# Kernel tuning notes

Hardware: AMD Instinct MI355X
Metric: run time of the kernel (lower is better)

The kernel has to match this reference:

```python
import jax, jax.numpy as jnp
import numpy as np

N = 100_000      # nodes
E = 1_600_000    # edges
D = 128          # in_dim == hidden_dim
H = 4            # heads
HD = D // H      # per-head dim = 32
B = 8            # graphs in batch
TD = 128         # time_dim
NEG_SLOPE = 0.2
EPS = 1e-5


def _gelu(v):
    return jax.nn.gelu(v, approximate=False)  # torch default erf-GELU


def _layernorm(v, g, b):
    mu = jnp.mean(v, axis=-1, keepdims=True)
    var = jnp.var(v, axis=-1, keepdims=True)
    return (v - mu) * jax.lax.rsqrt(var + EPS) * g + b


def setup_inputs() -> dict:
    key = jax.random.key(0)
    ks = jax.random.split(key, 24)
    s = 1.0 / np.sqrt(D)
    inp = {
        "x": jax.random.normal(ks[0], (N, D), jnp.float32),
        "src": jax.random.randint(ks[1], (E,), 0, N),
        "dst": jax.random.randint(ks[2], (E,), 0, N),
        "graph_ids": jnp.sort(jax.random.randint(ks[3], (N,), 0, B)),
        "time_emb": jax.random.normal(ks[4], (B, TD), jnp.float32),
        # GATv2 params
        "Wsrc": jax.random.normal(ks[5], (D, D), jnp.float32) * s,
        "bsrc": jnp.zeros((D,), jnp.float32),
        "Wdst": jax.random.normal(ks[6], (D, D), jnp.float32) * s,
        "bdst": jnp.zeros((D,), jnp.float32),
        "attn": jax.random.normal(ks[7], (H, HD), jnp.float32) * (1.0 / np.sqrt(HD)),
        "gat_bias": jnp.zeros((D,), jnp.float32),
        # LayerNorms
        "ln1_g": jnp.ones((D,), jnp.float32), "ln1_b": jnp.zeros((D,), jnp.float32),
        "ln2_g": jnp.ones((D,), jnp.float32), "ln2_b": jnp.zeros((D,), jnp.float32),
        # time MLP
        "tW": jax.random.normal(ks[8], (TD, D), jnp.float32) * (1.0 / np.sqrt(TD)),
        "tb": jnp.zeros((D,), jnp.float32),
        # FFN
        "W1": jax.random.normal(ks[9], (D, 2 * D), jnp.float32) * s,
        "b1": jnp.zeros((2 * D,), jnp.float32),
        "W2": jax.random.normal(ks[10], (2 * D, D), jnp.float32) * (1.0 / np.sqrt(2 * D)),
        "b2": jnp.zeros((D,), jnp.float32),
    }
    return inp


def reference(x, src, dst, graph_ids, time_emb, Wsrc, bsrc, Wdst, bdst, attn,
              gat_bias, ln1_g, ln1_b, ln2_g, ln2_b, tW, tb, W1, b1, W2, b2):
    h = _layernorm(x, ln1_g, ln1_b)                       # [N, D]
    # GATv2Conv (share_weights=False, residual=False, activation=gelu)
    feat_src = (h @ Wsrc + bsrc).reshape(N, H, HD)        # [N, H, HD]
    feat_dst = (h @ Wdst + bdst).reshape(N, H, HD)
    e = feat_src[src] + feat_dst[dst]                     # [E, H, HD]
    e = jnp.where(e > 0, e, NEG_SLOPE * e)                # leaky_relu
    scores = jnp.einsum("ehd,hd->eh", e, attn)            # [E, H]
    # segment softmax over incoming edges of each dst node
    m = jax.ops.segment_max(scores, dst, num_segments=N)  # [N, H]
    ex = jnp.exp(scores - m[dst])
    denom = jax.ops.segment_sum(ex, dst, num_segments=N)  # [N, H]
    alpha = ex / denom[dst]                               # [E, H]
    msg = feat_src[src] * alpha[:, :, None]               # [E, H, HD]
    rst = jax.ops.segment_sum(msg, dst, num_segments=N)   # [N, H, HD]
    rst = _gelu(rst + gat_bias.reshape(H, HD))
    h = rst.reshape(N, D)                                 # flatten(1)
    # ragged time-embedding expand: time_condition[graph_of(node)]
    time_cond = _gelu(time_emb @ tW + tb)                 # [B, D]
    h = h + time_cond[graph_ids]
    h = h + x                                             # proj = Identity (in_dim == hidden_dim)
    h2 = _layernorm(h, ln2_g, ln2_b)
    h2 = _gelu(h2 @ W1 + b1) @ W2 + b2                    # FFN
    return h + h2
```

## Files before the change

### kernel.cpp

```cpp
#include <hip/hip_runtime.h>
#include <hip/hip_bf16.h>


#define RB 16
#define NEG_SLOPE 0.2f
#define LN_EPS 1e-5f

typedef __attribute__((ext_vector_type(8))) short short8v;
typedef __attribute__((ext_vector_type(4))) float floatx4;
typedef __attribute__((ext_vector_type(2))) float f32x2;

__device__ __forceinline__ float gelu_erf(float v) {
    return 0.5f * v * (1.0f + erff(v * 0.70710678118654752f));
}
__device__ __forceinline__ unsigned short f2bf(float f) {
    unsigned int u = __float_as_uint(f);
    u += 0x7fffu + ((u >> 16) & 1u);
    return (unsigned short)(u >> 16);
}
__device__ __forceinline__ float bf2f(unsigned short u) {
    return __uint_as_float(((unsigned int)u) << 16);
}

__device__ __forceinline__ void pack_region(
    const float* __restrict__ W, unsigned short* __restrict__ P, int K, int C, int idx)
{
    int total = (K >> 5) * (C >> 4) * 64;
    if (idx >= total) return;
    int lane = idx & 63;
    int f = idx >> 6;
    int nkt = K >> 5;
    int nt = f / nkt, kt = f - nt * nkt;
    int col = nt * 16 + (lane & 15);
    int k0 = kt * 32 + 8 * (lane >> 4);
    short8v v;
    #pragma unroll
    for (int i = 0; i < 8; ++i)
        v[i] = (short)f2bf(W[(size_t)(k0 + i) * C + col]);
    *(short8v*)(P + (size_t)idx * 8) = v;
}

__global__ __launch_bounds__(256) void prep(
    const int* __restrict__ dst, int* __restrict__ deg, int* __restrict__ rank,
    int E, int nRank,
    const float* __restrict__ temb, const float* __restrict__ tW,
    const float* __restrict__ tb, float* __restrict__ tc, int B,
    const float* __restrict__ Wsrc, unsigned short* __restrict__ pWs,
    const float* __restrict__ Wdst, unsigned short* __restrict__ pWd,
    const float* __restrict__ W1,   unsigned short* __restrict__ pW1,
    const float* __restrict__ W2,   unsigned short* __restrict__ pW2)
{
    const int t = threadIdx.x;
    if (blockIdx.x < nRank) {
        int e = blockIdx.x * 256 + t;
        if (e < E) rank[e] = atomicAdd(&deg[dst[e]], 1);
        return;
    }
    const int bid = blockIdx.x - nRank;
    if (bid == 0) {
        __shared__ float te[8 * 128];
        for (int i = t; i < B * 128; i += 256) te[i] = temb[i];
        __syncthreads();
        int c = t & 127, half = t >> 7;
        for (int b = half * 4; b < half * 4 + 4; ++b) {
            if (b >= B) break;
            float acc = 0.f;
            for (int k = 0; k < 128; ++k) acc = fmaf(te[b * 128 + k], tW[k * 128 + c], acc);
            tc[b * 128 + c] = gelu_erf(acc + tb[c]);
        }
    } else if (bid < 9) {
        pack_region(Wsrc, pWs, 128, 128, (bid - 1) * 256 + t);
    } else if (bid < 17) {
        pack_region(Wdst, pWd, 128, 128, (bid - 9) * 256 + t);
    } else if (bid < 33) {
        pack_region(W1, pW1, 128, 256, (bid - 17) * 256 + t);
    } else {
        pack_region(W2, pW2, 256, 128, (bid - 33) * 256 + t);
    }
}

__global__ __launch_bounds__(256) void scan_blocks(
    const int* __restrict__ deg, int* __restrict__ rs, int* __restrict__ btot, int N)
{
    __shared__ int wtot[4];
    const int t    = threadIdx.x;
    const int idx  = blockIdx.x * 1024 + t * 4;
    int d0 = 0, d1 = 0, d2 = 0, d3 = 0;
    if (idx + 3 < N) {
        int4 v = *(const int4*)(deg + idx);
        d0 = v.x; d1 = v.y; d2 = v.z; d3 = v.w;
    } else {
        if (idx     < N) d0 = deg[idx];
        if (idx + 1 < N) d1 = deg[idx + 1];
        if (idx + 2 < N) d2 = deg[idx + 2];
        if (idx + 3 < N) d3 = deg[idx + 3];
    }
    const int ts = d0 + d1 + d2 + d3;
    const int lane = t & 63, w = t >> 6;
    int incl = ts;
    #pragma unroll
    for (int m = 1; m < 64; m <<= 1) { int u = __shfl_up(incl, m); if (lane >= m) incl += u; }
    if (lane == 63) wtot[w] = incl;
    __syncthreads();
    int woff = 0;
    #pragma unroll
    for (int i = 0; i < 4; ++i) woff += (i < w) ? wtot[i] : 0;
    const int p = woff + incl - ts;
    if (idx + 3 < N) {
        int4 o;
        o.x = p; o.y = p + d0; o.z = p + d0 + d1; o.w = p + d0 + d1 + d2;
        *(int4*)(rs + idx) = o;
    } else {
        if (idx     < N) rs[idx]     = p;
        if (idx + 1 < N) rs[idx + 1] = p + d0;
        if (idx + 2 < N) rs[idx + 2] = p + d0 + d1;
        if (idx + 3 < N) rs[idx + 3] = p + d0 + d1 + d2;
    }
    if (t == 255) btot[blockIdx.x] = woff + incl;
}

__global__ __launch_bounds__(64) void scan_tops(
    int* __restrict__ btot, int nb, int* __restrict__ rs, int N, int E)
{
    const int lane = threadIdx.x;
    int a0 = (2 * lane     < nb) ? btot[2 * lane]     : 0;
    int a1 = (2 * lane + 1 < nb) ? btot[2 * lane + 1] : 0;
    const int ts = a0 + a1;
    int incl = ts;
    #pragma unroll
    for (int m = 1; m < 64; m <<= 1) { int u = __shfl_up(incl, m); if (lane >= m) incl += u; }
    const int ex = incl - ts;
    if (2 * lane     < nb) btot[2 * lane]     = ex;
    if (2 * lane + 1 < nb) btot[2 * lane + 1] = ex + a0;
    if (lane == 0) rs[N] = E;
}

__global__ __launch_bounds__(256) void scan_add(
    int* __restrict__ rs, const int* __restrict__ btot, int N)
{
    int i = blockIdx.x * 256 + threadIdx.x;
    if (i < N) rs[i] += btot[i >> 10];
}

__global__ __launch_bounds__(256) void ln1_fill(
    const float* __restrict__ x,
    const float* __restrict__ ln_g, const float* __restrict__ ln_b,
    const unsigned short* __restrict__ pWs, const float* __restrict__ bsrc,
    const unsigned short* __restrict__ pWd, const float* __restrict__ bdst,
    unsigned short* __restrict__ fs, unsigned short* __restrict__ fdB, int nrows, int nLn1,
    const int* __restrict__ dst, const int* __restrict__ srcA,
    const int* __restrict__ rs, const int* __restrict__ rank,
    int* __restrict__ srcSorted, int E)
{
    __shared__ __align__(16) float hs[RB][132];
    __shared__ __align__(16) unsigned short pa[4 * 64 * 8];
    __shared__ float s_mu[RB], s_rs[RB];

    if (blockIdx.x >= nLn1) {
        int e = (blockIdx.x - nLn1) * 256 + threadIdx.x;
        if (e < E) srcSorted[rs[dst[e]] + rank[e]] = srcA[e];
        return;
    }

    const int tid  = threadIdx.x;
    const int row0 = blockIdx.x * RB;
    const int lane = tid & 63;
    const int w    = tid >> 6;

    #pragma unroll
    for (int i = 0; i < 2; ++i) {
        int f   = tid + i * 256;
        int row = f >> 5;
        int c0  = (f & 31) * 4;
        float4 v = make_float4(0.f, 0.f, 0.f, 0.f);
        if (row0 + row < nrows) v = *(const float4*)(x + (size_t)(row0 + row) * 128 + c0);
        *(float4*)&hs[row][c0] = v;
    }
    __syncthreads();

    {
        const int ln = lane;
        #pragma unroll
        for (int rr = 0; rr < 4; ++rr) {
            int row = w * 4 + rr;
            float v0 = hs[row][ln * 2], v1 = hs[row][ln * 2 + 1];
            float s = v0 + v1, sq = v0 * v0 + v1 * v1;
            #pragma unroll
            for (int m = 32; m; m >>= 1) { s += __shfl_xor(s, m); sq += __shfl_xor(sq, m); }
            if (ln == 0) {
                float mu  = s * (1.0f / 128.0f);
                float var = sq * (1.0f / 128.0f) - mu * mu;
                s_mu[row] = mu;
                s_rs[row] = rsqrtf(var + LN_EPS);
            }
        }
    }
    __syncthreads();

    {
        const int kt  = w;
        const int row = lane & 15;
        const int k0  = kt * 32 + 8 * (lane >> 4);
        float mu = s_mu[row], rs2 = s_rs[row];
        float4 u  = *(float4*)&hs[row][k0];
        float4 v  = *(float4*)&hs[row][k0 + 4];
        float4 g0 = *(const float4*)&ln_g[k0];
        float4 g1 = *(const float4*)&ln_g[k0 + 4];
        float4 c0 = *(const float4*)&ln_b[k0];
        float4 c1 = *(const float4*)&ln_b[k0 + 4];
        short8v pv;
        pv[0] = (short)f2bf((u.x - mu) * rs2 * g0.x + c0.x);
        pv[1] = (short)f2bf((u.y - mu) * rs2 * g0.y + c0.y);
        pv[2] = (short)f2bf((u.z - mu) * rs2 * g0.z + c0.z);
        pv[3] = (short)f2bf((u.w - mu) * rs2 * g0.w + c0.w);
        pv[4] = (short)f2bf((v.x - mu) * rs2 * g1.x + c1.x);
        pv[5] = (short)f2bf((v.y - mu) * rs2 * g1.y + c1.y);
        pv[6] = (short)f2bf((v.z - mu) * rs2 * g1.z + c1.z);
        pv[7] = (short)f2bf((v.w - mu) * rs2 * g1.w + c1.w);
        *(short8v*)&pa[(kt * 64 + lane) * 8] = pv;
    }
    __syncthreads();

    short8v a[4];
    #pragma unroll
    for (int kt = 0; kt < 4; ++kt)
        a[kt] = *(const short8v*)&pa[(kt * 64 + lane) * 8];

    #pragma unroll
    for (int j = 0; j < 2; ++j) {
        const int nt = 2 * w + j;
        floatx4 aS = {0.f, 0.f, 0.f, 0.f};
        floatx4 aD = {0.f, 0.f, 0.f, 0.f};
        #pragma unroll
        for (int kt = 0; kt < 4; ++kt) {
            short8v bS = *(const short8v*)(pWs + (size_t)((nt * 4 + kt) * 64 + lane) * 8);
            aS = __builtin_amdgcn_mfma_f32_16x16x32_bf16(a[kt], bS, aS, 0, 0, 0);
            short8v bD = *(const short8v*)(pWd + (size_t)((nt * 4 + kt) * 64 + lane) * 8);
            aD = __builtin_amdgcn_mfma_f32_16x16x32_bf16(a[kt], bD, aD, 0, 0, 0);
        }
        const int col = nt * 16 + (lane & 15);
        const float bS0 = bsrc[col], bD0 = bdst[col];
        #pragma unroll
        for (int r = 0; r < 4; ++r) {
            int grow = row0 + 4 * (lane >> 4) + r;
            if (grow < nrows) {
                fs [(size_t)grow * 128 + col] = f2bf(aS[r] + bS0);
                fdB[(size_t)grow * 128 + col] = f2bf(aD[r] + bD0);
            }
        }
    }
}

__global__ __launch_bounds__(256) void gat_gather(
    const unsigned short* __restrict__ fs, const unsigned short* __restrict__ fdB,
    unsigned short* __restrict__ hm, const float* __restrict__ x,
    const int* __restrict__ srcSorted, const int* __restrict__ rs,
    const float* __restrict__ attn, const float* __restrict__ gat_bias,
    const int* __restrict__ gid, const float* __restrict__ tc, int N)
{
    const int lane = threadIdx.x & 63;
    const int wib  = threadIdx.x >> 6;
    const int n    = blockIdx.x * 4 + wib;
    if (n >= N) return;

    const int g   = lane >> 4;
    const int l16 = lane & 15;
    const int d0  = l16 * 8;

    f32x2 c1v[4], c2v[4], vdv[4];
    {
        float4 a0 = *(const float4*)(attn + d0);
        float4 a1 = *(const float4*)(attn + d0 + 4);
        float av[8] = {a0.x, a0.y, a0.z, a0.w, a1.x, a1.y, a1.z, a1.w};
        uint4 vdu = *(const uint4*)(fdB + (size_t)n * 128 + d0);
        unsigned int uu[4] = {vdu.x, vdu.y, vdu.z, vdu.w};
        #pragma unroll
        for (int j = 0; j < 4; ++j) {
            c1v[j].x = 0.6f * av[2 * j];     c1v[j].y = 0.6f * av[2 * j + 1];
            c2v[j].x = 0.4f * av[2 * j];     c2v[j].y = 0.4f * av[2 * j + 1];
            vdv[j].x = __uint_as_float(uu[j] << 16);
            vdv[j].y = __uint_as_float(uu[j] & 0xffff0000u);
        }
    }

    const int lo = rs[n], hi = rs[n + 1];
    const int T  = (hi - lo + 3) >> 2;

    float den = 0.f;
    f32x2 wv[4] = {{0.f, 0.f}, {0.f, 0.f}, {0.f, 0.f}, {0.f, 0.f}};

    int i = lo + g;
    bool vA = (i < hi);
    int sA = vA ? srcSorted[i] : 0;
    uint4 rA = *(const uint4*)(fs + (size_t)sA * 128 + d0);

    for (int t = 0; t < T; ++t) {
        const int inx = i + 4;
        const bool vB = (inx < hi);
        const int sB = vB ? srcSorted[inx] : 0;
        uint4 rB = *(const uint4*)(fs + (size_t)sB * 128 + d0);

        unsigned int ru[4] = {rA.x, rA.y, rA.z, rA.w};
        f32x2 v2[4];
        #pragma unroll
        for (int j = 0; j < 4; ++j) {
            v2[j].x = __uint_as_float(ru[j] << 16);
            v2[j].y = __uint_as_float(ru[j] & 0xffff0000u);
        }

        f32x2 p2 = {0.f, 0.f};
        #pragma unroll
        for (int j = 0; j < 4; ++j) {
            f32x2 e = v2[j] + vdv[j];
            p2 = __builtin_elementwise_fma(c1v[j], e, p2);
            p2 = __builtin_elementwise_fma(c2v[j],
                     __builtin_elementwise_abs(e), p2);
        }
        float p = p2.x + p2.y;
        p += __shfl_xor(p, 1);
        p += __shfl_xor(p, 2);
        float exv = vA ? __expf(p) : 0.f;
        den += exv;
        f32x2 ex2; ex2.x = exv; ex2.y = exv;
        #pragma unroll
        for (int j = 0; j < 4; ++j)
            wv[j] = __builtin_elementwise_fma(ex2, v2[j], wv[j]);

        vA = vB; rA = rB; i = inx;
    }

    float w[8];
    #pragma unroll
    for (int j = 0; j < 4; ++j) { w[2 * j] = wv[j].x; w[2 * j + 1] = wv[j].y; }

    den += __shfl_xor(den, 16);
    den += __shfl_xor(den, 32);
    #pragma unroll
    for (int j = 0; j < 8; ++j) {
        w[j] += __shfl_xor(w[j], 16);
        w[j] += __shfl_xor(w[j], 32);
    }

    if (g == 0) {
        const float inv = den > 0.f ? 1.0f / den : 0.f;
        const int gg = gid[n];
        float4 x0 = *(const float4*)(x  + (size_t)n * 128 + d0);
        float4 x1 = *(const float4*)(x  + (size_t)n * 128 + d0 + 4);
        float4 t0 = *(const float4*)(tc + (size_t)gg * 128 + d0);
        float4 t1 = *(const float4*)(tc + (size_t)gg * 128 + d0 + 4);
        float4 g0 = *(const float4*)(gat_bias + d0);
        float4 g1 = *(const float4*)(gat_bias + d0 + 4);
        float o[8];
        o[0] = gelu_erf(w[0] * inv + g0.x) + t0.x + x0.x;
        o[1] = gelu_erf(w[1] * inv + g0.y) + t0.y + x0.y;
        o[2] = gelu_erf(w[2] * inv + g0.z) + t0.z + x0.z;
        o[3] = gelu_erf(w[3] * inv + g0.w) + t0.w + x0.w;
        o[4] = gelu_erf(w[4] * inv + g1.x) + t1.x + x1.x;
        o[5] = gelu_erf(w[5] * inv + g1.y) + t1.y + x1.y;
        o[6] = gelu_erf(w[6] * inv + g1.z) + t1.z + x1.z;
        o[7] = gelu_erf(w[7] * inv + g1.w) + t1.w + x1.w;
        uint4 pk;
        pk.x = (unsigned int)f2bf(o[0]) | ((unsigned int)f2bf(o[1]) << 16);
        pk.y = (unsigned int)f2bf(o[2]) | ((unsigned int)f2bf(o[3]) << 16);
        pk.z = (unsigned int)f2bf(o[4]) | ((unsigned int)f2bf(o[5]) << 16);
        pk.w = (unsigned int)f2bf(o[6]) | ((unsigned int)f2bf(o[7]) << 16);
        *(uint4*)(hm + (size_t)n * 128 + d0) = pk;
    }
}

__global__ __launch_bounds__(256) void combine_ffn(
    const unsigned short* __restrict__ hmg,
    const float* __restrict__ ln_g, const float* __restrict__ ln_b,
    const unsigned short* __restrict__ pW1, const float* __restrict__ b1,
    const unsigned short* __restrict__ pW2, const float* __restrict__ b2,
    float* __restrict__ out, int nrows)
{
    __shared__ __align__(16) float hs[RB][132];
    __shared__ __align__(16) unsigned short pa[4 * 64 * 8];
    __shared__ __align__(16) unsigned short a2[RB * 264];
    __shared__ float s_mu[RB], s_rs[RB];

    const int tid  = threadIdx.x;
    const int row0 = blockIdx.x * RB;
    const int lane = tid & 63;
    const int w    = tid >> 6;

    {
        int row = tid >> 4;
        int c0  = (tid & 15) * 8;
        uint4 u = make_uint4(0, 0, 0, 0);
        if (row0 + row < nrows) u = *(const uint4*)(hmg + (size_t)(row0 + row) * 128 + c0);
        float* hr = &hs[row][c0];
        hr[0] = __uint_as_float(u.x << 16);
        hr[1] = __uint_as_float(u.x & 0xffff0000u);
        hr[2] = __uint_as_float(u.y << 16);
        hr[3] = __uint_as_float(u.y & 0xffff0000u);
        hr[4] = __uint_as_float(u.z << 16);
        hr[5] = __uint_as_float(u.z & 0xffff0000u);
        hr[6] = __uint_as_float(u.w << 16);
        hr[7] = __uint_as_float(u.w & 0xffff0000u);
    }
    __syncthreads();

    {
        const int ln = lane;
        #pragma unroll
        for (int rr = 0; rr < 4; ++rr) {
            int row = w * 4 + rr;
            float v0 = hs[row][ln * 2], v1 = hs[row][ln * 2 + 1];
            float s = v0 + v1, sq = v0 * v0 + v1 * v1;
            #pragma unroll
            for (int m = 32; m; m >>= 1) { s += __shfl_xor(s, m); sq += __shfl_xor(sq, m); }
            if (ln == 0) {
                float mu  = s * (1.0f / 128.0f);
                float var = sq * (1.0f / 128.0f) - mu * mu;
                s_mu[row] = mu;
                s_rs[row] = rsqrtf(var + LN_EPS);
            }
        }
    }
    __syncthreads();

    {
        const int kt  = w;
        const int row = lane & 15;
        const int k0  = kt * 32 + 8 * (lane >> 4);
        float mu = s_mu[row], rs2 = s_rs[row];
        float4 u  = *(float4*)&hs[row][k0];
        float4 v  = *(float4*)&hs[row][k0 + 4];
        float4 g0 = *(const float4*)&ln_g[k0];
        float4 g1 = *(const float4*)&ln_g[k0 + 4];
        float4 c0 = *(const float4*)&ln_b[k0];
        float4 c1 = *(const float4*)&ln_b[k0 + 4];
        short8v pv;
        pv[0] = (short)f2bf((u.x - mu) * rs2 * g0.x + c0.x);
        pv[1] = (short)f2bf((u.y - mu) * rs2 * g0.y + c0.y);
        pv[2] = (short)f2bf((u.z - mu) * rs2 * g0.z + c0.z);
        pv[3] = (short)f2bf((u.w - mu) * rs2 * g0.w + c0.w);
        pv[4] = (short)f2bf((v.x - mu) * rs2 * g1.x + c1.x);
        pv[5] = (short)f2bf((v.y - mu) * rs2 * g1.y + c1.y);
        pv[6] = (short)f2bf((v.z - mu) * rs2 * g1.z + c1.z);
        pv[7] = (short)f2bf((v.w - mu) * rs2 * g1.w + c1.w);
        *(short8v*)&pa[(kt * 64 + lane) * 8] = pv;
    }
    __syncthreads();

    {
        short8v a[4];
        #pragma unroll
        for (int kt = 0; kt < 4; ++kt)
            a[kt] = *(const short8v*)&pa[(kt * 64 + lane) * 8];

        #pragma unroll
        for (int jj = 0; jj < 4; ++jj) {
            const int nt = 4 * w + jj;
            floatx4 acc = {0.f, 0.f, 0.f, 0.f};
            #pragma unroll
            for (int kt = 0; kt < 4; ++kt) {
                short8v b = *(const short8v*)(pW1 + (size_t)((nt * 4 + kt) * 64 + lane) * 8);
                acc = __builtin_amdgcn_mfma_f32_16x16x32_bf16(a[kt], b, acc, 0, 0, 0);
            }
            const int col = nt * 16 + (lane & 15);
            const float bb = b1[col];
            #pragma unroll
            for (int r = 0; r < 4; ++r) {
                int rowD = 4 * (lane >> 4) + r;
                a2[rowD * 264 + col] = f2bf(gelu_erf(acc[r] + bb));
            }
        }
    }
    __syncthreads();

    {
        floatx4 acc2[2] = {{0.f, 0.f, 0.f, 0.f}, {0.f, 0.f, 0.f, 0.f}};
        #pragma unroll
        for (int kt = 0; kt < 8; ++kt) {
            short8v af = *(const short8v*)&a2[(lane & 15) * 264 + kt * 32 + 8 * (lane >> 4)];
            #pragma unroll
            for (int j = 0; j < 2; ++j) {
                const int nt = 2 * w + j;
                short8v b = *(const short8v*)(pW2 + (size_t)((nt * 8 + kt) * 64 + lane) * 8);
                acc2[j] = __builtin_amdgcn_mfma_f32_16x16x32_bf16(af, b, acc2[j], 0, 0, 0);
            }
        }
        #pragma unroll
        for (int j = 0; j < 2; ++j) {
            const int col = (2 * w + j) * 16 + (lane & 15);
            const float bb = b2[col];
            #pragma unroll
            for (int r = 0; r < 4; ++r) {
                int rowD = 4 * (lane >> 4) + r;
                int grow = row0 + rowD;
                if (grow < nrows)
                    out[(size_t)grow * 128 + col] = hs[rowD][col] + acc2[j][r] + bb;
            }
        }
    }
}

extern "C" void kernel_launch(void* const* d_in, const int* in_sizes, int n_in,
                              void* d_out, int out_size, void* d_ws, size_t ws_size,
                              hipStream_t stream)
{
    const float* x    = (const float*)d_in[0];
    const int*   src  = (const int*)  d_in[1];
    const int*   dst  = (const int*)  d_in[2];
    const int*   gid  = (const int*)  d_in[3];
    const float* temb = (const float*)d_in[4];
    const float* Wsrc = (const float*)d_in[5];
    const float* bsrc = (const float*)d_in[6];
    const float* Wdst = (const float*)d_in[7];
    const float* bdst = (const float*)d_in[8];
    const float* attn = (const float*)d_in[9];
    const float* gbias= (const float*)d_in[10];
    const float* ln1g = (const float*)d_in[11];
    const float* ln1b = (const float*)d_in[12];
    const float* ln2g = (const float*)d_in[13];
    const float* ln2b = (const float*)d_in[14];
    const float* tW   = (const float*)d_in[15];
    const float* tb   = (const float*)d_in[16];
    const float* W1   = (const float*)d_in[17];
    const float* b1   = (const float*)d_in[18];
    const float* W2   = (const float*)d_in[19];
    const float* b2   = (const float*)d_in[20];

    const int N = in_sizes[0] / 128;
    const int E = in_sizes[1];
    const int B = in_sizes[4] / 128;
    float* out = (float*)d_out;

    char* ws = (char*)d_ws;
    size_t off = 0;
    auto alloc = [&](size_t bytes) { void* p = ws + off; off += (bytes + 255) & ~(size_t)255; return p; };
    unsigned short* fs  = (unsigned short*)alloc((size_t)N * 128 * 2);
    unsigned short* fdB = (unsigned short*)alloc((size_t)N * 128 * 2);
    unsigned short* hm  = (unsigned short*)alloc((size_t)N * 128 * 2);
    int*   deg          = (int*)           alloc((size_t)N * 4);
    int*   rsb          = (int*)           alloc((size_t)(N + 1) * 4);
    int*   rank         = (int*)           alloc((size_t)E * 4);
    int*   srcSorted    = (int*)           alloc((size_t)E * 4);
    float* tc           = (float*)         alloc((size_t)B * 128 * 4);
    int*   btot         = (int*)           alloc((size_t)1024 * 4);
    unsigned short* pWs = (unsigned short*)alloc((size_t)128 * 128 * 2);
    unsigned short* pWd = (unsigned short*)alloc((size_t)128 * 128 * 2);
    unsigned short* pW1 = (unsigned short*)alloc((size_t)128 * 256 * 2);
    unsigned short* pW2 = (unsigned short*)alloc((size_t)256 * 128 * 2);

    const int nbScan = (N + 1023) >> 10;
    const int nRank  = (E + 255) / 256;
    const int nLn1   = (N + RB - 1) / RB;
    const int nFill  = (E + 255) / 256;

    hipMemsetAsync(deg, 0, (size_t)N * 4, stream);
    prep<<<nRank + 49, 256, 0, stream>>>(dst, deg, rank, E, nRank,
        temb, tW, tb, tc, B, Wsrc, pWs, Wdst, pWd, W1, pW1, W2, pW2);
    scan_blocks<<<nbScan, 256, 0, stream>>>(deg, rsb, btot, N);
    scan_tops<<<1, 64, 0, stream>>>(btot, nbScan, rsb, N, E);
    scan_add<<<(N + 255) / 256, 256, 0, stream>>>(rsb, btot, N);
    ln1_fill<<<nLn1 + nFill, 256, 0, stream>>>(
        x, ln1g, ln1b, pWs, bsrc, pWd, bdst, fs, fdB, N, nLn1,
        dst, src, rsb, rank, srcSorted, E);
    gat_gather<<<(N + 3) / 4, 256, 0, stream>>>(
        fs, fdB, hm, x, srcSorted, rsb, attn, gbias, gid, tc, N);
    combine_ffn<<<(N + RB - 1) / RB, 256, 0, stream>>>(
        hm, ln2g, ln2b, pW1, b1, pW2, b2, out, N);
}
```

Before: 264.1 us.

## Store GAT features head-major and gather per head to shrink random-read working set

Projected source/destination features are now written in a head-major [H][N][32] layout, and the gather kernel assigns one wavefront per (head, node) pair, processing 8 edges at a time with 64-bit loads. Each head pass touches only a quarter-size feature array, which is meant to improve L2/MALL hit rates for the random source-row gathers. The ln1_fill launch also interleaves LN/projection blocks with scatter-fill blocks. The cost is that edge indices and row offsets are read four times, there are more wavefronts, and global stores from the projection become strided.

```diff
diff --git a/kernel.cpp b/kernel.cpp
--- a/kernel.cpp
+++ b/kernel.cpp
@@ -17,9 +17,6 @@
     unsigned int u = __float_as_uint(f);
     u += 0x7fffu + ((u >> 16) & 1u);
     return (unsigned short)(u >> 16);
-}
-__device__ __forceinline__ float bf2f(unsigned short u) {
-    return __uint_as_float(((unsigned int)u) << 16);
 }
 
 __device__ __forceinline__ void pack_region(
@@ -150,20 +147,32 @@
     unsigned short* __restrict__ fs, unsigned short* __restrict__ fdB, int nrows, int nLn1,
     const int* __restrict__ dst, const int* __restrict__ srcA,
     const int* __restrict__ rs, const int* __restrict__ rank,
-    int* __restrict__ srcSorted, int E)
+    int* __restrict__ srcSorted, int E, int nFill)
 {
     __shared__ __align__(16) float hs[RB][132];
     __shared__ __align__(16) unsigned short pa[4 * 64 * 8];
     __shared__ float s_mu[RB], s_rs[RB];
 
-    if (blockIdx.x >= nLn1) {
-        int e = (blockIdx.x - nLn1) * 256 + threadIdx.x;
+    const int nPair = 2 * (nLn1 < nFill ? nLn1 : nFill);
+    bool isFill;
+    int idx;
+    if ((int)blockIdx.x < nPair) {
+        isFill = (blockIdx.x & 1);
+        idx = blockIdx.x >> 1;
+    } else {
+        int r = blockIdx.x - nPair;
+        isFill = (nFill > nLn1);
+        idx = (nLn1 < nFill ? nLn1 : nFill) + r;
+    }
+
+    if (isFill) {
+        int e = idx * 256 + threadIdx.x;
         if (e < E) srcSorted[rs[dst[e]] + rank[e]] = srcA[e];
         return;
     }
 
     const int tid  = threadIdx.x;
-    const int row0 = blockIdx.x * RB;
+    const int row0 = idx * RB;
     const int lane = tid & 63;
     const int w    = tid >> 6;
 
@@ -239,13 +248,15 @@
             aD = __builtin_amdgcn_mfma_f32_16x16x32_bf16(a[kt], bD, aD, 0, 0, 0);
         }
         const int col = nt * 16 + (lane & 15);
+        const int hh  = col >> 5, hd = col & 31;
         const float bS0 = bsrc[col], bD0 = bdst[col];
         #pragma unroll
         for (int r = 0; r < 4; ++r) {
             int grow = row0 + 4 * (lane >> 4) + r;
             if (grow < nrows) {
-                fs [(size_t)grow * 128 + col] = f2bf(aS[r] + bS0);
-                fdB[(size_t)grow * 128 + col] = f2bf(aD[r] + bD0);
+                size_t po = ((size_t)hh * nrows + grow) * 32 + hd;
+                fs [po] = f2bf(aS[r] + bS0);
+                fdB[po] = f2bf(aD[r] + bD0);
             }
         }
     }
@@ -260,57 +271,57 @@
 {
     const int lane = threadIdx.x & 63;
     const int wib  = threadIdx.x >> 6;
-    const int n    = blockIdx.x * 4 + wib;
-    if (n >= N) return;
-
-    const int g   = lane >> 4;
-    const int l16 = lane & 15;
-    const int d0  = l16 * 8;
-
-    f32x2 c1v[4], c2v[4], vdv[4];
-    {
-        float4 a0 = *(const float4*)(attn + d0);
-        float4 a1 = *(const float4*)(attn + d0 + 4);
-        float av[8] = {a0.x, a0.y, a0.z, a0.w, a1.x, a1.y, a1.z, a1.w};
-        uint4 vdu = *(const uint4*)(fdB + (size_t)n * 128 + d0);
-        unsigned int uu[4] = {vdu.x, vdu.y, vdu.z, vdu.w};
-        #pragma unroll
-        for (int j = 0; j < 4; ++j) {
-            c1v[j].x = 0.6f * av[2 * j];     c1v[j].y = 0.6f * av[2 * j + 1];
-            c2v[j].x = 0.4f * av[2 * j];     c2v[j].y = 0.4f * av[2 * j + 1];
-            vdv[j].x = __uint_as_float(uu[j] << 16);
-            vdv[j].y = __uint_as_float(uu[j] & 0xffff0000u);
-        }
+    const int wi   = blockIdx.x * 4 + wib;
+    if (wi >= N * 4) return;
+    const int h = wi / N;
+    const int n = wi - h * N;
+
+    const int g  = lane >> 3;
+    const int l8 = lane & 7;
+    const int d  = l8 * 4;
+
+    const size_t hb = (size_t)h * N;
+
+    f32x2 c1v[2], c2v[2], vdv[2];
+    {
+        float4 a4 = *(const float4*)(attn + h * 32 + d);
+        c1v[0].x = 0.6f * a4.x; c1v[0].y = 0.6f * a4.y;
+        c1v[1].x = 0.6f * a4.z; c1v[1].y = 0.6f * a4.w;
+        c2v[0].x = 0.4f * a4.x; c2v[0].y = 0.4f * a4.y;
+        c2v[1].x = 0.4f * a4.z; c2v[1].y = 0.4f * a4.w;
+        uint2 vdu = *(const uint2*)(fdB + (hb + n) * 32 + d);
+        vdv[0].x = __uint_as_float(vdu.x << 16);
+        vdv[0].y = __uint_as_float(vdu.x & 0xffff0000u);
+        vdv[1].x = __uint_as_float(vdu.y << 16);
+        vdv[1].y = __uint_as_float(vdu.y & 0xffff0000u);
     }
 
     const int lo = rs[n], hi = rs[n + 1];
-    const int T  = (hi - lo + 3) >> 2;
+    const int T  = (hi - lo + 7) >> 3;
 
     float den = 0.f;
-    f32x2 wv[4] = {{0.f, 0.f}, {0.f, 0.f}, {0.f, 0.f}, {0.f, 0.f}};
+    f32x2 wv[2] = {{0.f, 0.f}, {0.f, 0.f}};
 
     int i = lo + g;
     bool vA = (i < hi);
     int sA = vA ? srcSorted[i] : 0;
-    uint4 rA = *(const uint4*)(fs + (size_t)sA * 128 + d0);
+    uint2 rA = *(const uint2*)(fs + (hb + sA) * 32 + d);
 
     for (int t = 0; t < T; ++t) {
-        const int inx = i + 4;
+        const int inx = i + 8;
         const bool vB = (inx < hi);
         const int sB = vB ? srcSorted[inx] : 0;
-        uint4 rB = *(const uint4*)(fs + (size_t)sB * 128 + d0);
-
-        unsigned int ru[4] = {rA.x, rA.y, rA.z, rA.w};
-        f32x2 v2[4];
-        #pragma unroll
-        for (int j = 0; j < 4; ++j) {
-            v2[j].x = __uint_as_float(ru[j] << 16);
-            v2[j].y = __uint_as_float(ru[j] & 0xffff0000u);
-        }
+        uint2 rB = *(const uint2*)(fs + (hb + sB) * 32 + d);
+
+        f32x2 v2[2];
+        v2[0].x = __uint_as_float(rA.x << 16);
+        v2[0].y = __uint_as_float(rA.x & 0xffff0000u);
+        v2[1].x = __uint_as_float(rA.y << 16);
+        v2[1].y = __uint_as_float(rA.y & 0xffff0000u);
 
         f32x2 p2 = {0.f, 0.f};
         #pragma unroll
-        for (int j = 0; j < 4; ++j) {
+        for (int j = 0; j < 2; ++j) {
             f32x2 e = v2[j] + vdv[j];
             p2 = __builtin_elementwise_fma(c1v[j], e, p2);
             p2 = __builtin_elementwise_fma(c2v[j],
@@ -319,52 +330,39 @@
         float p = p2.x + p2.y;
         p += __shfl_xor(p, 1);
         p += __shfl_xor(p, 2);
+        p += __shfl_xor(p, 4);
         float exv = vA ? __expf(p) : 0.f;
         den += exv;
         f32x2 ex2; ex2.x = exv; ex2.y = exv;
-        #pragma unroll
-        for (int j = 0; j < 4; ++j)
-            wv[j] = __builtin_elementwise_fma(ex2, v2[j], wv[j]);
+        wv[0] = __builtin_elementwise_fma(ex2, v2[0], wv[0]);
+        wv[1] = __builtin_elementwise_fma(ex2, v2[1], wv[1]);
 
         vA = vB; rA = rB; i = inx;
     }
 
-    float w[8];
-    #pragma unroll
-    for (int j = 0; j < 4; ++j) { w[2 * j] = wv[j].x; w[2 * j + 1] = wv[j].y; }
-
-    den += __shfl_xor(den, 16);
-    den += __shfl_xor(den, 32);
-    #pragma unroll
-    for (int j = 0; j < 8; ++j) {
-        w[j] += __shfl_xor(w[j], 16);
-        w[j] += __shfl_xor(w[j], 32);
-    }
+    float w0 = wv[0].x, w1 = wv[0].y, w2 = wv[1].x, w3 = wv[1].y;
+
+    den += __shfl_xor(den, 8);  den += __shfl_xor(den, 16); den += __shfl_xor(den, 32);
+    w0  += __shfl_xor(w0, 8);   w0  += __shfl_xor(w0, 16);  w0  += __shfl_xor(w0, 32);
+    w1  += __shfl_xor(w1, 8);   w1  += __shfl_xor(w1, 16);  w1  += __shfl_xor(w1, 32);
+    w2  += __shfl_xor(w2, 8);   w2  += __shfl_xor(w2, 16);  w2  += __shfl_xor(w2, 32);
+    w3  += __shfl_xor(w3, 8);   w3  += __shfl_xor(w3, 16);  w3  += __shfl_xor(w3, 32);
 
     if (g == 0) {
         const float inv = den > 0.f ? 1.0f / den : 0.f;
         const int gg = gid[n];
-        float4 x0 = *(const float4*)(x  + (size_t)n * 128 + d0);
-        float4 x1 = *(const float4*)(x  + (size_t)n * 128 + d0 + 4);
-        float4 t0 = *(const float4*)(tc + (size_t)gg * 128 + d0);
-        float4 t1 = *(const float4*)(tc + (size_t)gg * 128 + d0 + 4);
-        float4 g0 = *(const float4*)(gat_bias + d0);
-        float4 g1 = *(const float4*)(gat_bias + d0 + 4);
-        float o[8];
-        o[0] = gelu_erf(w[0] * inv + g0.x) + t0.x + x0.x;
-        o[1] = gelu_erf(w[1] * inv + g0.y) + t0.y + x0.y;
-        o[2] = gelu_erf(w[2] * inv + g0.z) + t0.z + x0.z;
-        o[3] = gelu_erf(w[3] * inv + g0.w) + t0.w + x0.w;
-        o[4] = gelu_erf(w[4] * inv + g1.x) + t1.x + x1.x;
-        o[5] = gelu_erf(w[5] * inv + g1.y) + t1.y + x1.y;
-        o[6] = gelu_erf(w[6] * inv + g1.z) + t1.z + x1.z;
-        o[7] = gelu_erf(w[7] * inv + g1.w) + t1.w + x1.w;
-        uint4 pk;
-        pk.x = (unsigned int)f2bf(o[0]) | ((unsigned int)f2bf(o[1]) << 16);
-        pk.y = (unsigned int)f2bf(o[2]) | ((unsigned int)f2bf(o[3]) << 16);
-        pk.z = (unsigned int)f2bf(o[4]) | ((unsigned int)f2bf(o[5]) << 16);
-        pk.w = (unsigned int)f2bf(o[6]) | ((unsigned int)f2bf(o[7]) << 16);
-        *(uint4*)(hm + (size_t)n * 128 + d0) = pk;
+        const int c0 = h * 32 + d;
+        float4 x4 = *(const float4*)(x  + (size_t)n * 128 + c0);
+        float4 t4 = *(const float4*)(tc + (size_t)gg * 128 + c0);
+        float4 g4 = *(const float4*)(gat_bias + c0);
+        float o0 = gelu_erf(w0 * inv + g4.x) + t4.x + x4.x;
+        float o1 = gelu_erf(w1 * inv + g4.y) + t4.y + x4.y;
+        float o2 = gelu_erf(w2 * inv + g4.z) + t4.z + x4.z;
+        float o3 = gelu_erf(w3 * inv + g4.w) + t4.w + x4.w;
+        uint2 pk;
+        pk.x = (unsigned int)f2bf(o0) | ((unsigned int)f2bf(o1) << 16);
+        pk.y = (unsigned int)f2bf(o2) | ((unsigned int)f2bf(o3) << 16);
+        *(uint2*)(hm + (size_t)n * 128 + c0) = pk;
     }
 }
 
@@ -559,8 +557,8 @@
     scan_add<<<(N + 255) / 256, 256, 0, stream>>>(rsb, btot, N);
     ln1_fill<<<nLn1 + nFill, 256, 0, stream>>>(
         x, ln1g, ln1b, pWs, bsrc, pWd, bdst, fs, fdB, N, nLn1,
-        dst, src, rsb, rank, srcSorted, E);
-    gat_gather<<<(N + 3) / 4, 256, 0, stream>>>(
+        dst, src, rsb, rank, srcSorted, E, nFill);
+    gat_gather<<<(N * 4 + 3) / 4, 256, 0, stream>>>(
         fs, fdB, hm, x, srcSorted, rsb, attn, gbias, gid, tc, N);
     combine_ffn<<<(N + RB - 1) / RB, 256, 0, stream>>>(
         hm, ln2g, ln2b, pW1, b1, pW2, b2, out, N);
```

Measured after the change: 386.9 us. 1.47x slower.
